# Optimization experiments

Measured on AMD Instinct MI355X. Metric: run time of the kernel, lower is better.

The kernel has to match this reference:

```python
import jax, jax.numpy as jnp
import numpy as np


def setup_inputs() -> dict:
    key = jax.random.key(0)
    kx, kq, kk, kv = jax.random.split(key, 4)
    B, S, F, D = 4, 4096, 512, 64
    x = jax.random.normal(kx, (B, S, F), dtype=jnp.float32)
    Wq = jax.random.normal(kq, (F, D), dtype=jnp.float32) * 0.05
    Wk = jax.random.normal(kk, (F, D), dtype=jnp.float32) * 0.05
    Wv = jax.random.normal(kv, (F, D), dtype=jnp.float32) * 0.05
    return {"x": x, "Wq": Wq, "Wk": Wk, "Wv": Wv}


def reference(x, Wq, Wk, Wv):
    # x: [B,S,F]; Wq/Wk/Wv: [F,D]
    q = jnp.einsum('bsf,fd->bsd', x, Wq)
    k = jnp.einsum('bsf,fd->bsd', x, Wk)
    v = jnp.einsum('bsf,fd->bsd', x, Wv)
    scale = 1.0 / jnp.sqrt(jnp.asarray(Wq.shape[-1], dtype=x.dtype))
    scores = jnp.einsum('bqd,bkd->bqk', q, k) * scale  # [B,S,S]
    weights = jax.nn.softmax(scores, axis=-1)
    return jnp.einsum('bqk,bkd->bqd', weights, v)
```

## Files before the change

### kernel.cpp

```cpp
#include <hip/hip_runtime.h>

constexpr int Bc = 4, Sc = 4096, Fc = 512, Dc = 64;
constexpr int SPLIT = 4;
constexpr int KT = 64;
constexpr int TILES = (Sc / SPLIT) / KT;

typedef __attribute__((ext_vector_type(8)))  short  short8;
typedef __attribute__((ext_vector_type(4)))  float  float4v;
typedef __attribute__((ext_vector_type(16))) float  float16v;

__device__ inline unsigned short f2bf(float f) {
    union { float f; unsigned u; } v; v.f = f;
    unsigned r = v.u + 0x7FFF + ((v.u >> 16) & 1);
    return (unsigned short)(r >> 16);
}
__device__ inline unsigned pk2(float a, float b) {
    union { float f; unsigned u; } x, y; x.f = a; y.f = b;
    unsigned ra = x.u + 0x7FFF + ((x.u >> 16) & 1);
    unsigned rb = y.u + 0x7FFF + ((y.u >> 16) & 1);
    return (ra >> 16) | (rb & 0xFFFF0000u);
}
__device__ inline float exp2fast(float x) {
#if defined(__has_builtin) && __has_builtin(__builtin_amdgcn_exp2f)
    return __builtin_amdgcn_exp2f(x);
#else
    return __expf(x * 0.69314718055994531f);
#endif
}

__global__ __launch_bounds__(256) void prep_kernel(
    const float* __restrict__ Wq, const float* __restrict__ Wk,
    const float* __restrict__ Wv, unsigned short* __restrict__ Wf)
{
    int wi = blockIdx.x * 256 + threadIdx.x;
    int lane = wi & 63;
    int kc = (wi >> 6) & 15;
    int nt = wi >> 10;
    int lm = lane & 15, quad = lane >> 4;
    int n = nt * 16 + lm;
    const float* W = (n < 64) ? Wq : (n < 128) ? Wk : Wv;
    int nc = n & 63;
    float scale = (n < 64) ? 0.18033688011112042f : 1.0f;
    int kbase = kc * 32 + quad * 8;
    union { uint4 v; unsigned short s[8]; } tmp;
    #pragma unroll
    for (int j = 0; j < 8; ++j)
        tmp.s[j] = f2bf(W[(size_t)(kbase + j) * Dc + nc] * scale);
    *(uint4*)&Wf[(size_t)wi * 8] = tmp.v;
}

__global__ __launch_bounds__(256) void qkv_kernel(
    const float* __restrict__ x, const unsigned short* __restrict__ Wf,
    unsigned short* __restrict__ Qb, unsigned short* __restrict__ Kb,
    unsigned short* __restrict__ Vtb)
{
    __shared__ __align__(16) unsigned short Xs[2][16][72];
    __shared__ __align__(16) unsigned short Ot[16][200];
    const int t = threadIdx.x;
    const int lane = t & 63, w = t >> 6;
    const int lm = lane & 15, quad = lane >> 4;
    const int row0 = blockIdx.x * 16;
    const int sr = t >> 4, sc4 = (t & 15) * 4;

    float4 xv;
    auto load_x = [&](int k0) {
        xv = *(const float4*)&x[(size_t)(row0 + sr) * Fc + k0 + sc4];
    };
    load_x(0);

    float4v acc[3];
    #pragma unroll
    for (int n = 0; n < 3; ++n) acc[n] = float4v{0.f, 0.f, 0.f, 0.f};

    int buf = 0;
    #pragma unroll
    for (int k0 = 0; k0 < Fc; k0 += 64, buf ^= 1) {
        uint2 pk;
        pk.x = pk2(xv.x, xv.y); pk.y = pk2(xv.z, xv.w);
        *(uint2*)&Xs[buf][sr][sc4] = pk;
        __syncthreads();
        if (k0 + 64 < Fc) load_x(k0 + 64);

        short8 af[2];
        #pragma unroll
        for (int h = 0; h < 2; ++h)
            af[h] = *(const short8*)&Xs[buf][lm][h * 32 + quad * 8];

        #pragma unroll
        for (int n = 0; n < 3; ++n) {
            const int nt = 3 * w + n;
            #pragma unroll
            for (int h = 0; h < 2; ++h) {
                const int kchunk = (k0 >> 5) + h;
                short8 bf_ = *(const short8*)&Wf[(size_t)((nt * 16 + kchunk) * 64 + lane) * 8];
                acc[n] = __builtin_amdgcn_mfma_f32_16x16x32_bf16(af[h], bf_, acc[n], 0, 0, 0);
            }
        }
    }

    __syncthreads();
    #pragma unroll
    for (int n = 0; n < 3; ++n)
        #pragma unroll
        for (int r = 0; r < 4; ++r)
            Ot[quad * 4 + r][(3 * w + n) * 16 + lm] = f2bf(acc[n][r]);
    __syncthreads();

    {
        const int r2 = t >> 4, c2 = (t & 15) * 4;
        *(uint2*)&Qb[(size_t)(row0 + r2) * Dc + c2] = *(const uint2*)&Ot[r2][c2];
        *(uint2*)&Kb[(size_t)(row0 + r2) * Dc + c2] = *(const uint2*)&Ot[r2][64 + c2];
    }
    {
        const int d = t >> 2, s4 = (t & 3) * 4;
        union { uint2 v; unsigned short s[4]; } tmp;
        #pragma unroll
        for (int j = 0; j < 4; ++j) tmp.s[j] = Ot[s4 + j][128 + d];
        const int bb = row0 >> 12, s0r = row0 & (Sc - 1);
        *(uint2*)&Vtb[((size_t)bb * Dc + d) * Sc + s0r + s4] = tmp.v;
    }
}

__global__ __launch_bounds__(256) void attn_kernel(
    const unsigned short* __restrict__ Qb, const unsigned short* __restrict__ Kb,
    const unsigned short* __restrict__ Vtb,
    float* __restrict__ Op, float* __restrict__ lp)
{
    constexpr int PD = 72;
    __shared__ __align__(16) char smem[36864];
    unsigned short* Kt = (unsigned short*)smem;
    unsigned short* Vt = (unsigned short*)(smem + 9216);
    unsigned short* Pt = (unsigned short*)(smem + 18432);

    const int t = threadIdx.x;
    const int lane = t & 63, w = t >> 6;
    const int l31 = lane & 31, lh = lane >> 5;
    const int b = blockIdx.y, z = blockIdx.z;
    const int q0 = blockIdx.x * 128 + w * 32;
    const size_t qkbase = (size_t)b * Sc * Dc;
    const size_t vbase  = (size_t)b * Dc * Sc;
    const int k0base = z * (Sc / SPLIT);

    short8 qf[4];
    #pragma unroll
    for (int c = 0; c < 4; ++c)
        qf[c] = *(const short8*)&Qb[qkbase + (size_t)(q0 + l31) * Dc + c * 16 + lh * 8];

    float16v O0, O1;
    #pragma unroll
    for (int r = 0; r < 16; ++r) { O0[r] = 0.f; O1[r] = 0.f; }
    float l_i = 0.f;

    const int skey = t >> 2, sd = (t & 3) * 16;
    uint4 kr[2], vr[2];
    auto load_tile = [&](int k0) {
        const unsigned short* kp = Kb + qkbase + (size_t)(k0 + skey) * Dc + sd;
        const unsigned short* vp = Vtb + vbase + (size_t)skey * Sc + k0 + sd;
        kr[0] = *(const uint4*)kp;  kr[1] = *(const uint4*)(kp + 8);
        vr[0] = *(const uint4*)vp;  vr[1] = *(const uint4*)(vp + 8);
    };
    load_tile(k0base);

    for (int kt = 0; kt < TILES; ++kt) {
        __syncthreads();
        *(uint4*)&Kt[skey * PD + sd]     = kr[0];
        *(uint4*)&Kt[skey * PD + sd + 8] = kr[1];
        *(uint4*)&Vt[skey * PD + sd]     = vr[0];
        *(uint4*)&Vt[skey * PD + sd + 8] = vr[1];
        __syncthreads();
        if (kt + 1 < TILES) load_tile(k0base + (kt + 1) * KT);

        float16v s0, s1;
        #pragma unroll
        for (int r = 0; r < 16; ++r) { s0[r] = 0.f; s1[r] = 0.f; }
        #pragma unroll
        for (int c = 0; c < 4; ++c) {
            short8 a0 = *(const short8*)&Kt[(l31) * PD + c * 16 + lh * 8];
            short8 a1 = *(const short8*)&Kt[(32 + l31) * PD + c * 16 + lh * 8];
            s0 = __builtin_amdgcn_mfma_f32_32x32x16_bf16(a0, qf[c], s0, 0, 0, 0);
            s1 = __builtin_amdgcn_mfma_f32_32x32x16_bf16(a1, qf[c], s1, 0, 0, 0);
        }

        #pragma unroll
        for (int r = 0; r < 16; ++r) {
            float p0 = exp2fast(s0[r]); s0[r] = p0; l_i += p0;
            float p1 = exp2fast(s1[r]); s1[r] = p1; l_i += p1;
        }

        unsigned short* prow = &Pt[w * 32 * PD + l31 * PD];
        #pragma unroll
        for (int g = 0; g < 4; ++g) {
            uint2 v;
            v.x = pk2(s0[4 * g], s0[4 * g + 1]); v.y = pk2(s0[4 * g + 2], s0[4 * g + 3]);
            *(uint2*)&prow[8 * g + 4 * lh] = v;
            v.x = pk2(s1[4 * g], s1[4 * g + 1]); v.y = pk2(s1[4 * g + 2], s1[4 * g + 3]);
            *(uint2*)&prow[32 + 8 * g + 4 * lh] = v;
        }

        #pragma unroll
        for (int c = 0; c < 4; ++c) {
            short8 pb  = *(const short8*)&prow[c * 16 + lh * 8];
            short8 va0 = *(const short8*)&Vt[(l31) * PD + c * 16 + lh * 8];
            short8 va1 = *(const short8*)&Vt[(32 + l31) * PD + c * 16 + lh * 8];
            O0 = __builtin_amdgcn_mfma_f32_32x32x16_bf16(va0, pb, O0, 0, 0, 0);
            O1 = __builtin_amdgcn_mfma_f32_32x32x16_bf16(va1, pb, O1, 0, 0, 0);
        }
    }

    l_i += __shfl_xor(l_i, 32);

    __syncthreads();
    float* Of = (float*)(smem + w * 8704);
    #pragma unroll
    for (int r = 0; r < 16; ++r) {
        int d0 = (r & 3) + 8 * (r >> 2) + 4 * lh;
        Of[l31 * 68 + d0]      = O0[r];
        Of[l31 * 68 + 32 + d0] = O1[r];
    }
    const size_t obase = ((size_t)(z * Bc + b) * Sc + q0) * Dc;
    const int qr = lane >> 4, c4 = (lane & 15) * 4;
    #pragma unroll
    for (int i = 0; i < 8; ++i) {
        int q = i * 4 + qr;
        *(float4*)&Op[obase + (size_t)q * Dc + c4] = *(const float4*)&Of[q * 68 + c4];
    }
    if (lane < 32)
        lp[(z * Bc + b) * Sc + q0 + l31] = l_i;
}

__global__ __launch_bounds__(256) void combine_kernel(
    const float* __restrict__ Op, const float* __restrict__ lp,
    float* __restrict__ out)
{
    const int BS = Bc * Sc;
    int tid = blockIdx.x * 256 + threadIdx.x;
    int bq = tid >> 4, dc = (tid & 15) * 4;
    float L = lp[bq] + lp[BS + bq] + lp[2 * BS + bq] + lp[3 * BS + bq];
    float inv = 1.f / L;
    size_t o = (size_t)bq * Dc + dc;
    size_t stride = (size_t)BS * Dc;
    float4 p0 = *(const float4*)&Op[o];
    float4 p1 = *(const float4*)&Op[o + stride];
    float4 p2 = *(const float4*)&Op[o + 2 * stride];
    float4 p3 = *(const float4*)&Op[o + 3 * stride];
    float4 r;
    r.x = (p0.x + p1.x + p2.x + p3.x) * inv;
    r.y = (p0.y + p1.y + p2.y + p3.y) * inv;
    r.z = (p0.z + p1.z + p2.z + p3.z) * inv;
    r.w = (p0.w + p1.w + p2.w + p3.w) * inv;
    *(float4*)&out[o] = r;
}

extern "C" void kernel_launch(void* const* d_in, const int* in_sizes, int n_in,
                              void* d_out, int out_size, void* d_ws, size_t ws_size,
                              hipStream_t stream) {
    const float* x  = (const float*)d_in[0];
    const float* Wq = (const float*)d_in[1];
    const float* Wk = (const float*)d_in[2];
    const float* Wv = (const float*)d_in[3];
    float* out = (float*)d_out;

    char* p = (char*)d_ws;
    unsigned short* Wf  = (unsigned short*)p;  p += (size_t)192 * Fc * 2;
    unsigned short* Qb  = (unsigned short*)p;  p += (size_t)Bc * Sc * Dc * 2;
    unsigned short* Kb  = (unsigned short*)p;  p += (size_t)Bc * Sc * Dc * 2;
    unsigned short* Vtb = (unsigned short*)p;  p += (size_t)Bc * Sc * Dc * 2;
    float* lp = (float*)p;                     p += (size_t)SPLIT * Bc * Sc * 4;
    float* Op = (float*)p;

    prep_kernel<<<48, 256, 0, stream>>>(Wq, Wk, Wv, Wf);
    qkv_kernel<<<Bc * Sc / 16, 256, 0, stream>>>(x, Wf, Qb, Kb, Vtb);
    attn_kernel<<<dim3(Sc / 128, Bc, SPLIT), 256, 0, stream>>>(Qb, Kb, Vtb, Op, lp);
    combine_kernel<<<(Bc * Sc * 16) / 256, 256, 0, stream>>>(Op, lp, out);
}
```

Before: 140.0 us.

## Fuse split-K combine into attention via atomic ticket and halve block size

```diff
diff --git a/kernel.cpp b/kernel.cpp
--- a/kernel.cpp
+++ b/kernel.cpp
@@ -30,9 +30,11 @@
 
 __global__ __launch_bounds__(256) void prep_kernel(
     const float* __restrict__ Wq, const float* __restrict__ Wk,
-    const float* __restrict__ Wv, unsigned short* __restrict__ Wf)
+    const float* __restrict__ Wv, unsigned short* __restrict__ Wf,
+    int* __restrict__ ticket)
 {
     int wi = blockIdx.x * 256 + threadIdx.x;
+    if (wi < 256) ticket[wi] = 0;
     int lane = wi & 63;
     int kc = (wi >> 6) & 15;
     int nt = wi >> 10;
@@ -121,22 +123,25 @@
     }
 }
 
-__global__ __launch_bounds__(256) void attn_kernel(
+__global__ __launch_bounds__(128) void attn_kernel(
     const unsigned short* __restrict__ Qb, const unsigned short* __restrict__ Kb,
     const unsigned short* __restrict__ Vtb,
-    float* __restrict__ Op, float* __restrict__ lp)
+    float* __restrict__ Op, float* __restrict__ lp,
+    int* __restrict__ ticket, float* __restrict__ out)
 {
     constexpr int PD = 72;
-    __shared__ __align__(16) char smem[36864];
+    __shared__ __align__(16) char smem[27648];
     unsigned short* Kt = (unsigned short*)smem;
     unsigned short* Vt = (unsigned short*)(smem + 9216);
     unsigned short* Pt = (unsigned short*)(smem + 18432);
+    __shared__ int s_old;
 
     const int t = threadIdx.x;
     const int lane = t & 63, w = t >> 6;
     const int l31 = lane & 31, lh = lane >> 5;
     const int b = blockIdx.y, z = blockIdx.z;
-    const int q0 = blockIdx.x * 128 + w * 32;
+    const int qt0 = blockIdx.x * 64;
+    const int q0 = qt0 + w * 32;
     const size_t qkbase = (size_t)b * Sc * Dc;
     const size_t vbase  = (size_t)b * Dc * Sc;
     const int k0base = z * (Sc / SPLIT);
@@ -151,22 +156,26 @@
     for (int r = 0; r < 16; ++r) { O0[r] = 0.f; O1[r] = 0.f; }
     float l_i = 0.f;
 
-    const int skey = t >> 2, sd = (t & 3) * 16;
-    uint4 kr[2], vr[2];
+    const int skey = t >> 1, sd = (t & 1) * 32;
+    uint4 kr[4], vr[4];
     auto load_tile = [&](int k0) {
         const unsigned short* kp = Kb + qkbase + (size_t)(k0 + skey) * Dc + sd;
         const unsigned short* vp = Vtb + vbase + (size_t)skey * Sc + k0 + sd;
-        kr[0] = *(const uint4*)kp;  kr[1] = *(const uint4*)(kp + 8);
-        vr[0] = *(const uint4*)vp;  vr[1] = *(const uint4*)(vp + 8);
+        #pragma unroll
+        for (int j = 0; j < 2; ++j) {
+            kr[j] = *(const uint4*)(kp + j * 8);   kr[j + 2] = *(const uint4*)(kp + 16 + j * 8);
+            vr[j] = *(const uint4*)(vp + j * 8);   vr[j + 2] = *(const uint4*)(vp + 16 + j * 8);
+        }
     };
     load_tile(k0base);
 
     for (int kt = 0; kt < TILES; ++kt) {
         __syncthreads();
-        *(uint4*)&Kt[skey * PD + sd]     = kr[0];
-        *(uint4*)&Kt[skey * PD + sd + 8] = kr[1];
-        *(uint4*)&Vt[skey * PD + sd]     = vr[0];
-        *(uint4*)&Vt[skey * PD + sd + 8] = vr[1];
+        #pragma unroll
+        for (int j = 0; j < 4; ++j) {
+            *(uint4*)&Kt[skey * PD + sd + j * 8] = kr[j];
+            *(uint4*)&Vt[skey * PD + sd + j * 8] = vr[j];
+        }
         __syncthreads();
         if (kt + 1 < TILES) load_tile(k0base + (kt + 1) * KT);
 
@@ -226,29 +235,59 @@
     }
     if (lane < 32)
         lp[(z * Bc + b) * Sc + q0 + l31] = l_i;
-}
-
-__global__ __launch_bounds__(256) void combine_kernel(
-    const float* __restrict__ Op, const float* __restrict__ lp,
-    float* __restrict__ out)
-{
-    const int BS = Bc * Sc;
-    int tid = blockIdx.x * 256 + threadIdx.x;
-    int bq = tid >> 4, dc = (tid & 15) * 4;
-    float L = lp[bq] + lp[BS + bq] + lp[2 * BS + bq] + lp[3 * BS + bq];
-    float inv = 1.f / L;
-    size_t o = (size_t)bq * Dc + dc;
-    size_t stride = (size_t)BS * Dc;
-    float4 p0 = *(const float4*)&Op[o];
-    float4 p1 = *(const float4*)&Op[o + stride];
-    float4 p2 = *(const float4*)&Op[o + 2 * stride];
-    float4 p3 = *(const float4*)&Op[o + 3 * stride];
-    float4 r;
-    r.x = (p0.x + p1.x + p2.x + p3.x) * inv;
-    r.y = (p0.y + p1.y + p2.y + p3.y) * inv;
-    r.z = (p0.z + p1.z + p2.z + p3.z) * inv;
-    r.w = (p0.w + p1.w + p2.w + p3.w) * inv;
-    *(float4*)&out[o] = r;
+
+    __syncthreads();
+    if (t == 0) {
+        __threadfence();
+        s_old = atomicAdd(&ticket[blockIdx.x * Bc + b], 1);
+    }
+    __syncthreads();
+    if (s_old == SPLIT - 1) {
+        __threadfence();
+        const int row = t >> 1, dh = (t & 1) * 32;
+        const size_t BSD = (size_t)Bc * Sc * Dc;
+        const size_t rbase = ((size_t)b * Sc + qt0 + row) * Dc + dh;
+        float acc[8] = {};
+        float L = 0.f;
+        #pragma unroll
+        for (int zz = 0; zz < SPLIT; ++zz) {
+            const float* src = Op + zz * BSD + rbase;
+            #pragma unroll
+            for (int j = 0; j < 8; ++j) {
+                float4 v = *(const float4*)(src + j * 4);
+                acc[j * 4 / 4] = acc[j];
+                acc[j] = acc[j];
+                ((float4*)acc)[0] = ((float4*)acc)[0];
+            }
+            #pragma unroll
+            for (int j = 0; j < 8; ++j) {
+                float4 v = *(const float4*)(src + j * 4);
+                acc[j] += v.x + 0.f;
+            }
+            L += lp[(zz * Bc + b) * Sc + qt0 + row];
+        }
+        float4 a[8];
+        #pragma unroll
+        for (int j = 0; j < 8; ++j) a[j] = make_float4(0.f, 0.f, 0.f, 0.f);
+        float L2 = 0.f;
+        #pragma unroll
+        for (int zz = 0; zz < SPLIT; ++zz) {
+            const float* src = Op + zz * BSD + rbase;
+            #pragma unroll
+            for (int j = 0; j < 8; ++j) {
+                float4 v = *(const float4*)(src + j * 4);
+                a[j].x += v.x; a[j].y += v.y; a[j].z += v.z; a[j].w += v.w;
+            }
+            L2 += lp[(zz * Bc + b) * Sc + qt0 + row];
+        }
+        float inv = 1.f / L2;
+        float* dst = out + rbase;
+        #pragma unroll
+        for (int j = 0; j < 8; ++j) {
+            float4 r = make_float4(a[j].x * inv, a[j].y * inv, a[j].z * inv, a[j].w * inv);
+            *(float4*)(dst + j * 4) = r;
+        }
+    }
 }
 
 extern "C" void kernel_launch(void* const* d_in, const int* in_sizes, int n_in,
@@ -266,10 +305,10 @@
     unsigned short* Kb  = (unsigned short*)p;  p += (size_t)Bc * Sc * Dc * 2;
     unsigned short* Vtb = (unsigned short*)p;  p += (size_t)Bc * Sc * Dc * 2;
     float* lp = (float*)p;                     p += (size_t)SPLIT * Bc * Sc * 4;
+    int* ticket = (int*)p;                     p += 4096;
     float* Op = (float*)p;
 
-    prep_kernel<<<48, 256, 0, stream>>>(Wq, Wk, Wv, Wf);
+    prep_kernel<<<48, 256, 0, stream>>>(Wq, Wk, Wv, Wf, ticket);
     qkv_kernel<<<Bc * Sc / 16, 256, 0, stream>>>(x, Wf, Qb, Kb, Vtb);
-    attn_kernel<<<dim3(Sc / 128, Bc, SPLIT), 256, 0, stream>>>(Qb, Kb, Vtb, Op, lp);
-    combine_kernel<<<(Bc * Sc * 16) / 256, 256, 0, stream>>>(Op, lp, out);
-}
+    attn_kernel<<<dim3(Sc / 64, Bc, SPLIT), 128, 0, stream>>>(Qb, Kb, Vtb, Op, lp, ticket, out);
+}
```

New measurement: 223.2 us. 59.4% more time.
